# Kernel tuning notes

Hardware: AMD Instinct MI355X
Metric: run time of the kernel (lower is better)

## Reference

```python
import jax, jax.numpy as jnp
import numpy as np

HID = 128
OUT = 128
NC = 100000
NA = 1024
FC = 256
FA = 4096

def _sage(x_src, x_dst, ei, Wl, bl, Wr):
    # PyG SAGEConv, mean aggregation, bipartite:
    # out[i] = lin_l(mean_{j->i} x_src[j]) + lin_r(x_dst[i])
    n_dst = x_dst.shape[0]
    src, dst = ei[0], ei[1]
    msg = x_src[src]                                  # [E, F_src] gather
    agg = jax.ops.segment_sum(msg, dst, num_segments=n_dst)
    cnt = jax.ops.segment_sum(jnp.ones((ei.shape[1],), x_src.dtype), dst, num_segments=n_dst)
    mean = agg / jnp.clip(cnt, 1.0, None)[:, None]
    return mean @ Wl.T + bl + x_dst @ Wr.T

def setup_inputs() -> dict:
    key = jax.random.key(0)
    ks = jax.random.split(key, 20)
    d = {}
    d["article_x"] = jax.random.normal(ks[0], (1, FA), jnp.float32)
    d["community_x"] = jax.random.normal(ks[1], (NC, FC), jnp.float32)
    # bipartite edges: row = article node idx (<NA), col = community idx (<NC)
    d["e_wb"] = jnp.stack([jax.random.randint(ks[2], (500000,), 0, NA, jnp.int32),
                            jax.random.randint(ks[3], (500000,), 0, NC, jnp.int32)])
    d["e_mb"] = jnp.stack([jax.random.randint(ks[4], (500000,), 0, NA, jnp.int32),
                            jax.random.randint(ks[5], (500000,), 0, NC, jnp.int32)])
    d["e_cc"] = jax.random.randint(ks[6], (2, 800000), 0, NC, jnp.int32)
    s = lambda k, sh: jax.random.normal(k, sh, jnp.float32) * (1.0 / np.sqrt(sh[-1]))
    d["W_lin1"] = s(ks[7], (NA, FA)); d["b_lin1"] = jnp.zeros((NA,), jnp.float32)
    d["Wl1"] = s(ks[8], (HID, 1));   d["bl1"] = jnp.zeros((HID,), jnp.float32); d["Wr1"] = s(ks[9], (HID, FC))
    d["Wl2"] = s(ks[10], (HID, 1));  d["bl2"] = jnp.zeros((HID,), jnp.float32); d["Wr2"] = s(ks[11], (HID, HID))
    d["Wl3"] = s(ks[12], (HID, HID)); d["bl3"] = jnp.zeros((HID,), jnp.float32); d["Wr3"] = s(ks[13], (HID, FC))
    d["W_lin2"] = s(ks[14], (OUT, HID)); d["b_lin2"] = jnp.zeros((OUT,), jnp.float32)
    d["Wd1"] = s(ks[15], (OUT, 2 * OUT)); d["bd1"] = jnp.zeros((OUT,), jnp.float32)
    d["Wd2"] = s(ks[16], (1, OUT)); d["bd2"] = jnp.zeros((1,), jnp.float32)
    return d

def reference(article_x, community_x, e_wb, e_mb, e_cc,
              W_lin1, b_lin1, Wl1, bl1, Wr1, Wl2, bl2, Wr2,
              Wl3, bl3, Wr3, W_lin2, b_lin2, Wd1, bd1, Wd2, bd2):
    # encoder
    art = (article_x @ W_lin1.T + b_lin1).reshape(NA, 1)      # [1024, 1]
    h1 = jax.nn.relu(_sage(art, community_x, e_wb, Wl1, bl1, Wr1))   # [NC, HID]
    h2 = jax.nn.relu(_sage(art, h1, e_mb, Wl2, bl2, Wr2))            # [NC, HID]
    h3 = jax.nn.relu(_sage(h2, community_x, e_cc, Wl3, bl3, Wr3))    # [NC, HID]
    z = h3 @ W_lin2.T + b_lin2                                       # [NC, OUT]
    # edge decoder on interacts_with edges
    row, col = e_cc[0], e_cc[1]
    zz = jnp.concatenate([z[row], z[col]], axis=-1)                  # [E, 2*OUT]
    h = jax.nn.relu(zz @ Wd1.T + bd1)
    return (h @ Wd2.T + bd2).reshape(-1)                             # [E]
```

## Files before the change

### kernel.cpp

```cpp
#include <hip/hip_runtime.h>

#define NC 100000
#define NA 1024
#define FA 4096

typedef _Float16 half8 __attribute__((ext_vector_type(8)));
typedef _Float16 half4v __attribute__((ext_vector_type(4)));
typedef _Float16 half2v __attribute__((ext_vector_type(2)));
typedef float floatx4 __attribute__((ext_vector_type(4)));

#define CNT_OFF 4294967296.0
#define CNT_INV 2.3283064365386963e-10

__device__ __forceinline__ void cvt_range(const float* __restrict__ in,
                                          _Float16* __restrict__ out, int n4,
                                          int bid, int nb) {
    int t = bid * 256 + threadIdx.x;
    int stride = nb * 256;
    for (int i = t; i < n4; i += stride) {
        float4 v = ((const float4*)in)[i];
        half4v h = {(_Float16)v.x, (_Float16)v.y, (_Float16)v.z, (_Float16)v.w};
        ((half4v*)out)[i] = h;
    }
}

__device__ __forceinline__ void edge_seg(const int* __restrict__ ei, int E,
                                         const float* __restrict__ art,
                                         double* __restrict__ acd, int bid, int nb) {
    int t = bid * 256 + threadIdx.x;
    int stride = nb * 256;
    for (int e = t; e < E; e += stride) {
        int s = ei[e], d = ei[E + e];
        atomicAdd(&acd[d], (double)art[s] + CNT_OFF);
    }
}

__device__ __forceinline__ void hist_seg(const int* __restrict__ ei, int E,
                                         int* __restrict__ deg, int bid, int nb) {
    int t = bid * 256 + threadIdx.x;
    int stride = nb * 256;
    for (int e = t; e < E; e += stride) atomicAdd(&deg[ei[E + e]], 1);
}

__device__ __forceinline__ void wcomb_seg(const float* __restrict__ Wd1,
                                          const float* __restrict__ Wlin2,
                                          _Float16* __restrict__ Wuh,
                                          _Float16* __restrict__ Wvh, int bid) {
    int i = bid * 2 + (threadIdx.x >> 7);
    int j = threadIdx.x & 127;
    float au = 0.f, av = 0.f;
    for (int m = 0; m < 128; ++m) {
        float wl = Wlin2[m * 128 + j];
        au = fmaf(Wd1[i * 256 + m], wl, au);
        av = fmaf(Wd1[i * 256 + 128 + m], wl, av);
    }
    Wuh[i * 128 + j] = (_Float16)au;
    Wvh[i * 128 + j] = (_Float16)av;
}

__device__ __forceinline__ void bcomb_seg(const float* __restrict__ Wd1,
                                          const float* __restrict__ b2,
                                          const float* __restrict__ bd1,
                                          float* __restrict__ bu, float* __restrict__ bv) {
    int i = threadIdx.x;
    if (i >= 128) return;
    float su = 0.f, sv = 0.f;
    for (int m = 0; m < 128; ++m) {
        float b = b2[m];
        su = fmaf(Wd1[i * 256 + m], b, su);
        sv = fmaf(Wd1[i * 256 + 128 + m], b, sv);
    }
    bu[i] = su + bd1[i];
    bv[i] = sv;
}

#define FRONT_WB   1024
#define FRONT_MB   1024
#define FRONT_HIST 768
#define FRONT_WCVT 96
#define FRONT_WCOMB 64
#define FRONT_BCOMB 1
#define FRONT_CVT  8192
#define FRONT_TOTAL (FRONT_WB + FRONT_MB + FRONT_HIST + FRONT_WCVT + FRONT_WCOMB + FRONT_BCOMB + FRONT_CVT)

__global__ __launch_bounds__(256)
void k_front(const int* __restrict__ e_wb, int E1,
             const int* __restrict__ e_mb, int E2,
             const int* __restrict__ e_cc, int E3,
             const float* __restrict__ art,
             double* __restrict__ acd1, double* __restrict__ acd2,
             int* __restrict__ deg,
             const float* __restrict__ Wr1, _Float16* __restrict__ Wr1h,
             const float* __restrict__ Wr2, _Float16* __restrict__ Wr2h,
             const float* __restrict__ Wl3, _Float16* __restrict__ Wl3h,
             const float* __restrict__ Wr3, _Float16* __restrict__ Wr3h,
             const float* __restrict__ Wd1, const float* __restrict__ Wlin2,
             _Float16* __restrict__ Wuh, _Float16* __restrict__ Wvh,
             const float* __restrict__ b2, const float* __restrict__ bd1,
             float* __restrict__ bu, float* __restrict__ bv,
             const float* __restrict__ cx, _Float16* __restrict__ cxh)
{
    int b = blockIdx.x;
    if (b < FRONT_WB) { edge_seg(e_wb, E1, art, acd1, b, FRONT_WB); return; }
    b -= FRONT_WB;
    if (b < FRONT_MB) { edge_seg(e_mb, E2, art, acd2, b, FRONT_MB); return; }
    b -= FRONT_MB;
    if (b < FRONT_HIST) { hist_seg(e_cc, E3, deg, b, FRONT_HIST); return; }
    b -= FRONT_HIST;
    if (b < FRONT_WCVT) {
        if (b < 32) cvt_range(Wr1, Wr1h, 8192, b, 32);
        else if (b < 48) cvt_range(Wr2, Wr2h, 4096, b - 32, 16);
        else if (b < 64) cvt_range(Wl3, Wl3h, 4096, b - 48, 16);
        else cvt_range(Wr3, Wr3h, 8192, b - 64, 32);
        return;
    }
    b -= FRONT_WCVT;
    if (b < FRONT_WCOMB) { wcomb_seg(Wd1, Wlin2, Wuh, Wvh, b); return; }
    b -= FRONT_WCOMB;
    if (b < FRONT_BCOMB) { bcomb_seg(Wd1, b2, bd1, bu, bv); return; }
    b -= FRONT_BCOMB;
    cvt_range(cx, cxh, NC * 64, b, FRONT_CVT);
}

__global__ void k_art(const float* __restrict__ ax, const float* __restrict__ W,
                      const float* __restrict__ b, float* __restrict__ art) {
    int wave = (blockIdx.x * blockDim.x + threadIdx.x) >> 6;
    int lane = threadIdx.x & 63;
    if (wave >= NA) return;
    const float* wr = W + (size_t)wave * FA;
    float s = 0.f;
    #pragma unroll
    for (int i = 0; i < FA; i += 256) {
        float4 a  = *(const float4*)&ax[i + 4 * lane];
        float4 wv = *(const float4*)&wr[i + 4 * lane];
        s += a.x * wv.x + a.y * wv.y + a.z * wv.z + a.w * wv.w;
    }
    for (int off = 32; off; off >>= 1) s += __shfl_down(s, off);
    if (lane == 0) art[wave] = s + b[wave];
}

__global__ void k_scan1(const int* __restrict__ deg, int* __restrict__ pre,
                        int* __restrict__ blksum) {
    __shared__ int ts[256];
    int base = blockIdx.x * 1024 + threadIdx.x * 4;
    int v0 = 0, v1 = 0, v2 = 0, v3 = 0;
    if (base + 0 < NC) v0 = deg[base + 0];
    if (base + 1 < NC) v1 = deg[base + 1];
    if (base + 2 < NC) v2 = deg[base + 2];
    if (base + 3 < NC) v3 = deg[base + 3];
    int tsum = v0 + v1 + v2 + v3;
    ts[threadIdx.x] = tsum;
    __syncthreads();
    for (int off = 1; off < 256; off <<= 1) {
        int y = (threadIdx.x >= off) ? ts[threadIdx.x - off] : 0;
        __syncthreads();
        ts[threadIdx.x] += y;
        __syncthreads();
    }
    int excl = ts[threadIdx.x] - tsum;
    if (base + 0 < NC) pre[base + 0] = excl;
    if (base + 1 < NC) pre[base + 1] = excl + v0;
    if (base + 2 < NC) pre[base + 2] = excl + v0 + v1;
    if (base + 3 < NC) pre[base + 3] = excl + v0 + v1 + v2;
    if (threadIdx.x == 255) blksum[blockIdx.x] = ts[255];
}

__global__ void k_scan2(int* __restrict__ blksum, int NB) {
    __shared__ int ts[256];
    int v = (threadIdx.x < NB) ? blksum[threadIdx.x] : 0;
    ts[threadIdx.x] = v;
    __syncthreads();
    for (int off = 1; off < 256; off <<= 1) {
        int y = (threadIdx.x >= off) ? ts[threadIdx.x - off] : 0;
        __syncthreads();
        ts[threadIdx.x] += y;
        __syncthreads();
    }
    if (threadIdx.x < NB) blksum[threadIdx.x] = ts[threadIdx.x] - v;
}

__global__ void k_scan3(const int* __restrict__ pre, const int* __restrict__ blksum,
                        const int* __restrict__ deg, int* __restrict__ off,
                        int* __restrict__ cursor, float* __restrict__ cntf) {
    int i = blockIdx.x * blockDim.x + threadIdx.x;
    if (i < NC) {
        int o = pre[i] + blksum[i >> 10];
        off[i] = o;
        cursor[i] = o;
        cntf[i] = (float)deg[i];
    }
}

__device__ __forceinline__ float mean_from_packed(double t) {
    double cd = rint(t * CNT_INV);
    float sum = (float)(t - cd * CNT_OFF);
    float cc = (float)cd;
    cc = cc > 1.f ? cc : 1.f;
    return sum / cc;
}

__device__ __forceinline__
void enc12_body(_Float16* lds, int blk,
                const _Float16* __restrict__ cxh, const _Float16* __restrict__ Wr1h,
                const _Float16* __restrict__ Wr2h,
                const float* __restrict__ bl1, const double* __restrict__ acd1,
                const float* __restrict__ Wl1,
                const float* __restrict__ bl2, const double* __restrict__ acd2,
                const float* __restrict__ Wl2,
                _Float16* __restrict__ out, int N)
{
    _Float16* Bh  = lds;
    _Float16* Ah  = lds + 128 * 40;
    _Float16* h1t = lds + 128 * 40;

    const int t = threadIdx.x, lane = t & 63, w = t >> 6;
    const int rowbase = blk * 128;
    const bool isA = t < 128;
    const int rr = isA ? t : t - 128;
    const int fr = lane & 15;
    const int kq = (lane >> 4) << 3;

    floatx4 zero4 = {0.f, 0.f, 0.f, 0.f};
    floatx4 acc[2][8];
    #pragma unroll
    for (int i = 0; i < 2; ++i)
        #pragma unroll
        for (int cf = 0; cf < 8; ++cf) acc[i][cf] = zero4;

    float4 p0, p1, p2, p3;
    float4 zf = make_float4(0.f, 0.f, 0.f, 0.f);
    {
        bool ok = true; const _Float16* base;
        if (isA) { int row = rowbase + rr; ok = row < N; base = ok ? &cxh[(size_t)row * 256] : Ah; }
        else base = &Wr1h[(size_t)rr * 256];
        const float4* s4 = (const float4*)base;
        p0 = ok ? s4[0] : zf; p1 = ok ? s4[1] : zf; p2 = ok ? s4[2] : zf; p3 = ok ? s4[3] : zf;
    }
    for (int tile = 0; tile < 8; ++tile) {
        float4* dst = (float4*)(isA ? &Ah[rr * 40] : &Bh[rr * 40]);
        dst[0] = p0; dst[1] = p1; dst[2] = p2; dst[3] = p3;
        __syncthreads();
        if (tile < 7) {
            int ko = (tile + 1) << 5;
            bool ok = true; const _Float16* base;
            if (isA) { int row = rowbase + rr; ok = row < N; base = ok ? &cxh[(size_t)row * 256 + ko] : Ah; }
            else base = &Wr1h[(size_t)rr * 256 + ko];
            const float4* s4 = (const float4*)base;
            p0 = ok ? s4[0] : zf; p1 = ok ? s4[1] : zf; p2 = ok ? s4[2] : zf; p3 = ok ? s4[3] : zf;
        }
        half8 af0 = *(const half8*)&Ah[(w * 32 + fr) * 40 + kq];
        half8 af1 = *(const half8*)&Ah[(w * 32 + 16 + fr) * 40 + kq];
        #pragma unroll
        for (int cf = 0; cf < 8; ++cf) {
            half8 bf = *(const half8*)&Bh[(cf * 16 + fr) * 40 + kq];
            acc[0][cf] = __builtin_amdgcn_mfma_f32_16x16x32_f16(af0, bf, acc[0][cf], 0, 0, 0);
            acc[1][cf] = __builtin_amdgcn_mfma_f32_16x16x32_f16(af1, bf, acc[1][cf], 0, 0, 0);
        }
        __syncthreads();
    }

    {
        float blc[8], wlc[8];
        #pragma unroll
        for (int cf = 0; cf < 8; ++cf) { int col = cf * 16 + fr; blc[cf] = bl1[col]; wlc[cf] = Wl1[col]; }
        #pragma unroll
        for (int i = 0; i < 2; ++i) {
            #pragma unroll
            for (int j = 0; j < 4; ++j) {
                int lrow = w * 32 + i * 16 + ((lane >> 4) << 2) + j;
                int grow = rowbase + lrow;
                float m = 0.f;
                if (grow < N) m = mean_from_packed(acd1[grow]);
                #pragma unroll
                for (int cf = 0; cf < 8; ++cf) {
                    float v = acc[i][cf][j] + blc[cf] + m * wlc[cf];
                    v = fmaxf(v, 0.f);
                    h1t[lrow * 136 + cf * 16 + fr] = (_Float16)v;
                }
            }
        }
    }
    __syncthreads();

    #pragma unroll
    for (int i = 0; i < 2; ++i)
        #pragma unroll
        for (int cf = 0; cf < 8; ++cf) acc[i][cf] = zero4;
    if (!isA) {
        const float4* s4 = (const float4*)&Wr2h[(size_t)rr * 128];
        p0 = s4[0]; p1 = s4[1]; p2 = s4[2]; p3 = s4[3];
    }
    for (int tt = 0; tt < 4; ++tt) {
        if (!isA) { float4* d = (float4*)&Bh[rr * 40]; d[0] = p0; d[1] = p1; d[2] = p2; d[3] = p3; }
        __syncthreads();
        if (!isA && tt < 3) {
            const float4* s4 = (const float4*)&Wr2h[(size_t)rr * 128 + ((tt + 1) << 5)];
            p0 = s4[0]; p1 = s4[1]; p2 = s4[2]; p3 = s4[3];
        }
        half8 af0 = *(const half8*)&h1t[(w * 32 + fr) * 136 + (tt << 5) + kq];
        half8 af1 = *(const half8*)&h1t[(w * 32 + 16 + fr) * 136 + (tt << 5) + kq];
        #pragma unroll
        for (int cf = 0; cf < 8; ++cf) {
            half8 bf = *(const half8*)&Bh[(cf * 16 + fr) * 40 + kq];
            acc[0][cf] = __builtin_amdgcn_mfma_f32_16x16x32_f16(af0, bf, acc[0][cf], 0, 0, 0);
            acc[1][cf] = __builtin_amdgcn_mfma_f32_16x16x32_f16(af1, bf, acc[1][cf], 0, 0, 0);
        }
        __syncthreads();
    }

    {
        float blc[8], wlc[8];
        #pragma unroll
        for (int cf = 0; cf < 8; ++cf) { int col = cf * 16 + fr; blc[cf] = bl2[col]; wlc[cf] = Wl2[col]; }
        #pragma unroll
        for (int i = 0; i < 2; ++i) {
            #pragma unroll
            for (int j = 0; j < 4; ++j) {
                int grow = rowbase + w * 32 + i * 16 + ((lane >> 4) << 2) + j;
                if (grow < N) {
                    float m = mean_from_packed(acd2[grow]);
                    #pragma unroll
                    for (int cf = 0; cf < 8; ++cf) {
                        float v = acc[i][cf][j] + blc[cf] + m * wlc[cf];
                        v = fmaxf(v, 0.f);
                        out[(size_t)grow * 128 + cf * 16 + fr] = (_Float16)v;
                    }
                }
            }
        }
    }
}

#define MID_GB  ((NC + 127) / 128)
#define MID_SC  768

__global__ __launch_bounds__(256)
void k_mid(const _Float16* __restrict__ cxh, const _Float16* __restrict__ Wr1h,
           const _Float16* __restrict__ Wr2h,
           const float* __restrict__ bl1, const double* __restrict__ acd1,
           const float* __restrict__ Wl1,
           const float* __restrict__ bl2, const double* __restrict__ acd2,
           const float* __restrict__ Wl2,
           _Float16* __restrict__ out, int N,
           const int* __restrict__ e_cc, int E3,
           int* __restrict__ cursor, int2* __restrict__ se)
{
    __shared__ _Float16 lds[128 * 40 + 128 * 136];
    if (blockIdx.x < MID_GB) {
        enc12_body(lds, blockIdx.x, cxh, Wr1h, Wr2h, bl1, acd1, Wl1, bl2, acd2, Wl2, out, N);
        return;
    }
    int bid = blockIdx.x - MID_GB;
    int t = bid * 256 + threadIdx.x;
    int stride = MID_SC * 256;
    for (int e = t; e < E3; e += stride) {
        int s = e_cc[e], d = e_cc[E3 + e];
        int p = atomicAdd(&cursor[d], 1);
        se[p] = make_int2(s, e);
    }
}

__global__ __launch_bounds__(256)
void k_csr_agg_h(const int* __restrict__ off, const int* __restrict__ deg,
                 const int2* __restrict__ se, const _Float16* __restrict__ h,
                 _Float16* __restrict__ agg) {
    int node = (blockIdx.x * blockDim.x + threadIdx.x) >> 6;
    int lane = threadIdx.x & 63;
    if (node >= NC) return;
    int b = off[node], d = deg[node];
    int dm = d < 64 ? d : 64;
    int sj = 0;
    if (lane < dm) sj = se[b + lane].x;
    float sx = 0.f, sy = 0.f;
    #pragma unroll 4
    for (int j = 0; j < dm; ++j) {
        int src = __shfl(sj, j);
        half2v m = *(const half2v*)&h[(size_t)src * 128 + 2 * lane];
        sx += (float)m[0]; sy += (float)m[1];
    }
    for (int j = 64; j < d; ++j) {
        int src = se[b + j].x;
        half2v m = *(const half2v*)&h[(size_t)src * 128 + 2 * lane];
        sx += (float)m[0]; sy += (float)m[1];
    }
    half2v r = {(_Float16)sx, (_Float16)sy};
    *(half2v*)&agg[(size_t)node * 128 + 2 * lane] = r;
}

__global__ __launch_bounds__(256)
void k_enc3uv(const _Float16* __restrict__ aggh, const _Float16* __restrict__ Wl3h,
              const _Float16* __restrict__ cxh, const _Float16* __restrict__ Wr3h,
              const float* __restrict__ bl3, const float* __restrict__ rcnt,
              const _Float16* __restrict__ Wuh, const float* __restrict__ bu,
              const _Float16* __restrict__ Wvh, const float* __restrict__ bv,
              _Float16* __restrict__ uout, _Float16* __restrict__ vout, int N)
{
    __shared__ _Float16 lds[128 * 40 + 128 * 136];
    _Float16* Bh  = lds;
    _Float16* Ah  = lds + 128 * 40;
    _Float16* h3t = lds + 128 * 40;

    const int t = threadIdx.x, lane = t & 63, w = t >> 6;
    const int rowbase = blockIdx.x * 128;
    const bool isA = t < 128;
    const int rr = isA ? t : t - 128;
    const int fr = lane & 15;
    const int kq = (lane >> 4) << 3;

    floatx4 zero4 = {0.f, 0.f, 0.f, 0.f};
    floatx4 acc[2][8];
    #pragma unroll
    for (int i = 0; i < 2; ++i)
        #pragma unroll
        for (int cf = 0; cf < 8; ++cf) acc[i][cf] = zero4;

    float4 p0, p1, p2, p3;
    float4 zf = make_float4(0.f, 0.f, 0.f, 0.f);
    {
        bool ok = true; const _Float16* base;
        if (isA) { int row = rowbase + rr; ok = row < N; base = ok ? &aggh[(size_t)row * 128] : Ah; }
        else base = &Wl3h[(size_t)rr * 128];
        const float4* s4 = (const float4*)base;
        p0 = ok ? s4[0] : zf; p1 = ok ? s4[1] : zf; p2 = ok ? s4[2] : zf; p3 = ok ? s4[3] : zf;
    }
    for (int tile = 0; tile < 12; ++tile) {
        float4* dst = (float4*)(isA ? &Ah[rr * 40] : &Bh[rr * 40]);
        dst[0] = p0; dst[1] = p1; dst[2] = p2; dst[3] = p3;
        __syncthreads();
        if (tile < 11) {
            int tn = tile + 1;
            bool ok = true; const _Float16* base;
            if (tn < 4) {
                int ko = tn << 5;
                if (isA) { int row = rowbase + rr; ok = row < N; base = ok ? &aggh[(size_t)row * 128 + ko] : Ah; }
                else base = &Wl3h[(size_t)rr * 128 + ko];
            } else {
                int ko = (tn - 4) << 5;
                if (isA) { int row = rowbase + rr; ok = row < N; base = ok ? &cxh[(size_t)row * 256 + ko] : Ah; }
                else base = &Wr3h[(size_t)rr * 256 + ko];
            }
            const float4* s4 = (const float4*)base;
            p0 = ok ? s4[0] : zf; p1 = ok ? s4[1] : zf; p2 = ok ? s4[2] : zf; p3 = ok ? s4[3] : zf;
        }
        half8 af0 = *(const half8*)&Ah[(w * 32 + fr) * 40 + kq];
        half8 af1 = *(const half8*)&Ah[(w * 32 + 16 + fr) * 40 + kq];
        #pragma unroll
        for (int cf = 0; cf < 8; ++cf) {
            half8 bf = *(const half8*)&Bh[(cf * 16 + fr) * 40 + kq];
            acc[0][cf] = __builtin_amdgcn_mfma_f32_16x16x32_f16(af0, bf, acc[0][cf], 0, 0, 0);
            acc[1][cf] = __builtin_amdgcn_mfma_f32_16x16x32_f16(af1, bf, acc[1][cf], 0, 0, 0);
        }
        if (tile == 3) {
            #pragma unroll
            for (int i = 0; i < 2; ++i)
                #pragma unroll
                for (int j = 0; j < 4; ++j) {
                    int row = rowbase + w * 32 + i * 16 + ((lane >> 4) << 2) + j;
                    float c = (row < N) ? rcnt[row] : 1.f;
                    c = c > 1.f ? c : 1.f;
                    float inv = 1.f / c;
                    #pragma unroll
                    for (int cf = 0; cf < 8; ++cf) acc[i][cf][j] *= inv;
                }
        }
        __syncthreads();
    }

    {
        float blc[8];
        #pragma unroll
        for (int cf = 0; cf < 8; ++cf) blc[cf] = bl3[cf * 16 + fr];
        #pragma unroll
        for (int i = 0; i < 2; ++i) {
            #pragma unroll
            for (int j = 0; j < 4; ++j) {
                int lrow = w * 32 + i * 16 + ((lane >> 4) << 2) + j;
                #pragma unroll
                for (int cf = 0; cf < 8; ++cf) {
                    float v = acc[i][cf][j] + blc[cf];
                    v = fmaxf(v, 0.f);
                    h3t[lrow * 136 + cf * 16 + fr] = (_Float16)v;
                }
            }
        }
    }
    __syncthreads();

    for (int ph = 0; ph < 2; ++ph) {
        const _Float16* Wp = ph ? Wvh : Wuh;
        const float* bp = ph ? bv : bu;
        _Float16* op = ph ? vout : uout;
        #pragma unroll
        for (int i = 0; i < 2; ++i)
            #pragma unroll
            for (int cf = 0; cf < 8; ++cf) acc[i][cf] = zero4;
        if (!isA) {
            const float4* s4 = (const float4*)&Wp[(size_t)rr * 128];
            p0 = s4[0]; p1 = s4[1]; p2 = s4[2]; p3 = s4[3];
        }
        for (int tt = 0; tt < 4; ++tt) {
            if (!isA) { float4* d = (float4*)&Bh[rr * 40]; d[0] = p0; d[1] = p1; d[2] = p2; d[3] = p3; }
            __syncthreads();
            if (!isA && tt < 3) {
                const float4* s4 = (const float4*)&Wp[(size_t)rr * 128 + ((tt + 1) << 5)];
                p0 = s4[0]; p1 = s4[1]; p2 = s4[2]; p3 = s4[3];
            }
            half8 af0 = *(const half8*)&h3t[(w * 32 + fr) * 136 + (tt << 5) + kq];
            half8 af1 = *(const half8*)&h3t[(w * 32 + 16 + fr) * 136 + (tt << 5) + kq];
            #pragma unroll
            for (int cf = 0; cf < 8; ++cf) {
                half8 bf = *(const half8*)&Bh[(cf * 16 + fr) * 40 + kq];
                acc[0][cf] = __builtin_amdgcn_mfma_f32_16x16x32_f16(af0, bf, acc[0][cf], 0, 0, 0);
                acc[1][cf] = __builtin_amdgcn_mfma_f32_16x16x32_f16(af1, bf, acc[1][cf], 0, 0, 0);
            }
            __syncthreads();
        }
        float bc[8];
        #pragma unroll
        for (int cf = 0; cf < 8; ++cf) bc[cf] = bp[cf * 16 + fr];
        #pragma unroll
        for (int i = 0; i < 2; ++i) {
            #pragma unroll
            for (int j = 0; j < 4; ++j) {
                int grow = rowbase + w * 32 + i * 16 + ((lane >> 4) << 2) + j;
                if (grow < N) {
                    #pragma unroll
                    for (int cf = 0; cf < 8; ++cf)
                        op[(size_t)grow * 128 + cf * 16 + fr] = (_Float16)(acc[i][cf][j] + bc[cf]);
                }
            }
        }
    }
}

__global__ __launch_bounds__(256)
void k_decoder_h(const int* __restrict__ off, const int* __restrict__ deg,
                 const int2* __restrict__ se,
                 const _Float16* __restrict__ u, const _Float16* __restrict__ v,
                 const float* __restrict__ wd2, const float* __restrict__ bd2,
                 float* __restrict__ out) {
    int node = (blockIdx.x * blockDim.x + threadIdx.x) >> 6;
    if (node >= NC) return;
    int lane = threadIdx.x & 63;
    int g = lane >> 3, s = lane & 7;

    float wf[16], vf[16];
    #pragma unroll
    for (int q = 0; q < 16; ++q) wf[q] = wd2[s * 16 + q];
    {
        half8 va = *(const half8*)&v[(size_t)node * 128 + s * 16];
        half8 vb = *(const half8*)&v[(size_t)node * 128 + s * 16 + 8];
        #pragma unroll
        for (int q = 0; q < 8; ++q) { vf[q] = (float)va[q]; vf[8 + q] = (float)vb[q]; }
    }
    float bb = bd2[0];

    int b = off[node], d = deg[node];
    int dm = d < 64 ? d : 64;
    int sj = 0, ej = 0;
    if (lane < dm) { int2 p = se[b + lane]; sj = p.x; ej = p.y; }

    for (int jb = 0; jb < d; jb += 8) {
        int j = jb + g;
        float p = 0.f;
        int eid = 0;
        bool act = j < d;
        int src = 0;
        if (jb < 64) {
            src = __shfl(sj, j);
            eid = __shfl(ej, j);
        } else if (act) {
            int2 pr = se[b + j];
            src = pr.x; eid = pr.y;
        }
        if (act) {
            half8 ua = *(const half8*)&u[(size_t)src * 128 + s * 16];
            half8 ub = *(const half8*)&u[(size_t)src * 128 + s * 16 + 8];
            #pragma unroll
            for (int q = 0; q < 8; ++q) {
                p = fmaf(wf[q],     fmaxf((float)ua[q] + vf[q],     0.f), p);
                p = fmaf(wf[8 + q], fmaxf((float)ub[q] + vf[8 + q], 0.f), p);
            }
        }
        p += __shfl_xor(p, 1);
        p += __shfl_xor(p, 2);
        p += __shfl_xor(p, 4);
        if (act && s == 0) out[eid] = p + bb;
    }
}

extern "C" void kernel_launch(void* const* d_in, const int* in_sizes, int n_in,
                              void* d_out, int out_size, void* d_ws, size_t ws_size,
                              hipStream_t stream) {
    const float* article_x = (const float*)d_in[0];
    const float* cx     = (const float*)d_in[1];
    const int*   e_wb   = (const int*)d_in[2];
    const int*   e_mb   = (const int*)d_in[3];
    const int*   e_cc   = (const int*)d_in[4];
    const float* W_lin1 = (const float*)d_in[5];
    const float* b_lin1 = (const float*)d_in[6];
    const float* Wl1    = (const float*)d_in[7];
    const float* bl1    = (const float*)d_in[8];
    const float* Wr1    = (const float*)d_in[9];
    const float* Wl2    = (const float*)d_in[10];
    const float* bl2    = (const float*)d_in[11];
    const float* Wr2    = (const float*)d_in[12];
    const float* Wl3    = (const float*)d_in[13];
    const float* bl3    = (const float*)d_in[14];
    const float* Wr3    = (const float*)d_in[15];
    const float* W_lin2 = (const float*)d_in[16];
    const float* b_lin2 = (const float*)d_in[17];
    const float* Wd1    = (const float*)d_in[18];
    const float* bd1    = (const float*)d_in[19];
    const float* Wd2    = (const float*)d_in[20];
    const float* bd2    = (const float*)d_in[21];
    float* out = (float*)d_out;

    const int E1 = in_sizes[2] / 2;
    const int E2 = in_sizes[3] / 2;
    const int E3 = in_sizes[4] / 2;

    double* acd1 = (double*)d_ws;
    double* acd2 = acd1 + NC;
    float* ws = (float*)(acd2 + NC);
    size_t o = 0;
    float* art   = ws;      o += 1024;
    float* cnt3f = ws + o;  o += NC;
    float* buf   = ws + o;  o += 128;
    float* bvf   = ws + o;  o += 128;
    int* deg    = (int*)(ws + o); o += NC;
    int* pre    = (int*)(ws + o); o += NC;
    int* off    = (int*)(ws + o); o += NC;
    int* cursor = (int*)(ws + o); o += NC;
    int* blksum = (int*)(ws + o); o += 256;
    int2* se    = (int2*)(ws + o); o += 2 * 800000;
    _Float16* hws = (_Float16*)(ws + o);
    size_t ho = 0;
    _Float16* cxh    = hws + ho; ho += (size_t)NC * 256;
    _Float16* B1h    = hws + ho; ho += (size_t)NC * 128;
    _Float16* B2h    = hws + ho; ho += (size_t)NC * 128;
    _Float16* Wr1h   = hws + ho; ho += 128 * 256;
    _Float16* Wr2h   = hws + ho; ho += 128 * 128;
    _Float16* Wl3h   = hws + ho; ho += 128 * 128;
    _Float16* Wr3h   = hws + ho; ho += 128 * 256;
    _Float16* Wuh    = hws + ho; ho += 128 * 128;
    _Float16* Wvh    = hws + ho; ho += 128 * 128;

    hipMemsetAsync(acd1, 0, 2 * NC * sizeof(double), stream);
    hipMemsetAsync(deg, 0, NC * sizeof(int), stream);

    k_art<<<256, 256, 0, stream>>>(article_x, W_lin1, b_lin1, art);

    k_front<<<FRONT_TOTAL, 256, 0, stream>>>(
        e_wb, E1, e_mb, E2, e_cc, E3, art, acd1, acd2, deg,
        Wr1, Wr1h, Wr2, Wr2h, Wl3, Wl3h, Wr3, Wr3h,
        Wd1, W_lin2, Wuh, Wvh, b_lin2, bd1, buf, bvf, cx, cxh);

    const int NB = (NC + 1023) / 1024;
    k_scan1<<<NB, 256, 0, stream>>>(deg, pre, blksum);
    k_scan2<<<1, 256, 0, stream>>>(blksum, NB);
    k_scan3<<<(NC + 255) / 256, 256, 0, stream>>>(pre, blksum, deg, off, cursor, cnt3f);

    k_mid<<<MID_GB + MID_SC, 256, 0, stream>>>(
        cxh, Wr1h, Wr2h, bl1, acd1, Wl1, bl2, acd2, Wl2,
        B1h, NC, e_cc, E3, cursor, se);

    const int GW = (NC * 64 + 255) / 256;
    k_csr_agg_h<<<GW, 256, 0, stream>>>(off, deg, se, B1h, B2h);
    k_enc3uv<<<MID_GB, 256, 0, stream>>>(B2h, Wl3h, cxh, Wr3h,
                                         bl3, cnt3f, Wuh, buf, Wvh, bvf,
                                         B1h, B2h, NC);
    k_decoder_h<<<GW, 256, 0, stream>>>(off, deg, se, B1h, B2h, Wd2, bd2, out);
}
```

Before: 349.6 us.

## Regroup front kernels and schedule CSR scatter blocks first in mid kernel

```diff
diff --git a/kernel.cpp b/kernel.cpp
--- a/kernel.cpp
+++ b/kernel.cpp
@@ -74,57 +74,11 @@
     bv[i] = sv;
 }
 
-#define FRONT_WB   1024
-#define FRONT_MB   1024
-#define FRONT_HIST 768
-#define FRONT_WCVT 96
-#define FRONT_WCOMB 64
-#define FRONT_BCOMB 1
-#define FRONT_CVT  8192
-#define FRONT_TOTAL (FRONT_WB + FRONT_MB + FRONT_HIST + FRONT_WCVT + FRONT_WCOMB + FRONT_BCOMB + FRONT_CVT)
-
-__global__ __launch_bounds__(256)
-void k_front(const int* __restrict__ e_wb, int E1,
-             const int* __restrict__ e_mb, int E2,
-             const int* __restrict__ e_cc, int E3,
-             const float* __restrict__ art,
-             double* __restrict__ acd1, double* __restrict__ acd2,
-             int* __restrict__ deg,
-             const float* __restrict__ Wr1, _Float16* __restrict__ Wr1h,
-             const float* __restrict__ Wr2, _Float16* __restrict__ Wr2h,
-             const float* __restrict__ Wl3, _Float16* __restrict__ Wl3h,
-             const float* __restrict__ Wr3, _Float16* __restrict__ Wr3h,
-             const float* __restrict__ Wd1, const float* __restrict__ Wlin2,
-             _Float16* __restrict__ Wuh, _Float16* __restrict__ Wvh,
-             const float* __restrict__ b2, const float* __restrict__ bd1,
-             float* __restrict__ bu, float* __restrict__ bv,
-             const float* __restrict__ cx, _Float16* __restrict__ cxh)
-{
-    int b = blockIdx.x;
-    if (b < FRONT_WB) { edge_seg(e_wb, E1, art, acd1, b, FRONT_WB); return; }
-    b -= FRONT_WB;
-    if (b < FRONT_MB) { edge_seg(e_mb, E2, art, acd2, b, FRONT_MB); return; }
-    b -= FRONT_MB;
-    if (b < FRONT_HIST) { hist_seg(e_cc, E3, deg, b, FRONT_HIST); return; }
-    b -= FRONT_HIST;
-    if (b < FRONT_WCVT) {
-        if (b < 32) cvt_range(Wr1, Wr1h, 8192, b, 32);
-        else if (b < 48) cvt_range(Wr2, Wr2h, 4096, b - 32, 16);
-        else if (b < 64) cvt_range(Wl3, Wl3h, 4096, b - 48, 16);
-        else cvt_range(Wr3, Wr3h, 8192, b - 64, 32);
-        return;
-    }
-    b -= FRONT_WCVT;
-    if (b < FRONT_WCOMB) { wcomb_seg(Wd1, Wlin2, Wuh, Wvh, b); return; }
-    b -= FRONT_WCOMB;
-    if (b < FRONT_BCOMB) { bcomb_seg(Wd1, b2, bd1, bu, bv); return; }
-    b -= FRONT_BCOMB;
-    cvt_range(cx, cxh, NC * 64, b, FRONT_CVT);
-}
-
-__global__ void k_art(const float* __restrict__ ax, const float* __restrict__ W,
-                      const float* __restrict__ b, float* __restrict__ art) {
-    int wave = (blockIdx.x * blockDim.x + threadIdx.x) >> 6;
+__device__ __forceinline__ void art_seg(const float* __restrict__ ax,
+                                        const float* __restrict__ W,
+                                        const float* __restrict__ b,
+                                        float* __restrict__ art, int bid) {
+    int wave = (bid * 256 + threadIdx.x) >> 6;
     int lane = threadIdx.x & 63;
     if (wave >= NA) return;
     const float* wr = W + (size_t)wave * FA;
@@ -137,6 +91,64 @@
     }
     for (int off = 32; off; off >>= 1) s += __shfl_down(s, off);
     if (lane == 0) art[wave] = s + b[wave];
+}
+
+#define PRE_ART   256
+#define PRE_HIST  512
+#define PRE_WCVT  96
+#define PRE_WCOMB 64
+#define PRE_BCOMB 1
+#define PRE_CVT   4096
+#define PRE_TOTAL (PRE_ART + PRE_HIST + PRE_WCVT + PRE_WCOMB + PRE_BCOMB + PRE_CVT)
+
+__global__ __launch_bounds__(256)
+void k_pre(const float* __restrict__ ax, const float* __restrict__ W_lin1,
+           const float* __restrict__ b_lin1, float* __restrict__ art,
+           const int* __restrict__ e_cc, int E3, int* __restrict__ deg,
+           const float* __restrict__ Wr1, _Float16* __restrict__ Wr1h,
+           const float* __restrict__ Wr2, _Float16* __restrict__ Wr2h,
+           const float* __restrict__ Wl3, _Float16* __restrict__ Wl3h,
+           const float* __restrict__ Wr3, _Float16* __restrict__ Wr3h,
+           const float* __restrict__ Wd1, const float* __restrict__ Wlin2,
+           _Float16* __restrict__ Wuh, _Float16* __restrict__ Wvh,
+           const float* __restrict__ b2, const float* __restrict__ bd1,
+           float* __restrict__ bu, float* __restrict__ bv,
+           const float* __restrict__ cx, _Float16* __restrict__ cxh)
+{
+    int b = blockIdx.x;
+    if (b < PRE_ART) { art_seg(ax, W_lin1, b_lin1, art, b); return; }
+    b -= PRE_ART;
+    if (b < PRE_HIST) { hist_seg(e_cc, E3, deg, b, PRE_HIST); return; }
+    b -= PRE_HIST;
+    if (b < PRE_WCVT) {
+        if (b < 32) cvt_range(Wr1, Wr1h, 8192, b, 32);
+        else if (b < 48) cvt_range(Wr2, Wr2h, 4096, b - 32, 16);
+        else if (b < 64) cvt_range(Wl3, Wl3h, 4096, b - 48, 16);
+        else cvt_range(Wr3, Wr3h, 8192, b - 64, 32);
+        return;
+    }
+    b -= PRE_WCVT;
+    if (b < PRE_WCOMB) { wcomb_seg(Wd1, Wlin2, Wuh, Wvh, b); return; }
+    b -= PRE_WCOMB;
+    if (b < PRE_BCOMB) { bcomb_seg(Wd1, b2, bd1, bu, bv); return; }
+    b -= PRE_BCOMB;
+    cvt_range(cx, cxh, NC * 64, b, PRE_CVT);
+}
+
+#define EDG_WB 1024
+#define EDG_MB 1024
+#define EDG_TOTAL (EDG_WB + EDG_MB)
+
+__global__ __launch_bounds__(256)
+void k_edges(const int* __restrict__ e_wb, int E1,
+             const int* __restrict__ e_mb, int E2,
+             const float* __restrict__ art,
+             double* __restrict__ acd1, double* __restrict__ acd2)
+{
+    int b = blockIdx.x;
+    if (b < EDG_WB) { edge_seg(e_wb, E1, art, acd1, b, EDG_WB); return; }
+    b -= EDG_WB;
+    edge_seg(e_mb, E2, art, acd2, b, EDG_MB);
 }
 
 __global__ void k_scan1(const int* __restrict__ deg, int* __restrict__ pre,
@@ -331,8 +343,8 @@
     }
 }
 
+#define MID_SC  256
 #define MID_GB  ((NC + 127) / 128)
-#define MID_SC  768
 
 __global__ __launch_bounds__(256)
 void k_mid(const _Float16* __restrict__ cxh, const _Float16* __restrict__ Wr1h,
@@ -346,18 +358,18 @@
            int* __restrict__ cursor, int2* __restrict__ se)
 {
     __shared__ _Float16 lds[128 * 40 + 128 * 136];
-    if (blockIdx.x < MID_GB) {
-        enc12_body(lds, blockIdx.x, cxh, Wr1h, Wr2h, bl1, acd1, Wl1, bl2, acd2, Wl2, out, N);
+    if (blockIdx.x < MID_SC) {
+        int t = blockIdx.x * 256 + threadIdx.x;
+        int stride = MID_SC * 256;
+        #pragma unroll 4
+        for (int e = t; e < E3; e += stride) {
+            int s = e_cc[e], d = e_cc[E3 + e];
+            int p = atomicAdd(&cursor[d], 1);
+            se[p] = make_int2(s, e);
+        }
         return;
     }
-    int bid = blockIdx.x - MID_GB;
-    int t = bid * 256 + threadIdx.x;
-    int stride = MID_SC * 256;
-    for (int e = t; e < E3; e += stride) {
-        int s = e_cc[e], d = e_cc[E3 + e];
-        int p = atomicAdd(&cursor[d], 1);
-        se[p] = make_int2(s, e);
-    }
+    enc12_body(lds, blockIdx.x - MID_SC, cxh, Wr1h, Wr2h, bl1, acd1, Wl1, bl2, acd2, Wl2, out, N);
 }
 
 __global__ __launch_bounds__(256)
@@ -649,19 +661,20 @@
     hipMemsetAsync(acd1, 0, 2 * NC * sizeof(double), stream);
     hipMemsetAsync(deg, 0, NC * sizeof(int), stream);
 
-    k_art<<<256, 256, 0, stream>>>(article_x, W_lin1, b_lin1, art);
-
-    k_front<<<FRONT_TOTAL, 256, 0, stream>>>(
-        e_wb, E1, e_mb, E2, e_cc, E3, art, acd1, acd2, deg,
+    k_pre<<<PRE_TOTAL, 256, 0, stream>>>(
+        article_x, W_lin1, b_lin1, art,
+        e_cc, E3, deg,
         Wr1, Wr1h, Wr2, Wr2h, Wl3, Wl3h, Wr3, Wr3h,
         Wd1, W_lin2, Wuh, Wvh, b_lin2, bd1, buf, bvf, cx, cxh);
+
+    k_edges<<<EDG_TOTAL, 256, 0, stream>>>(e_wb, E1, e_mb, E2, art, acd1, acd2);
 
     const int NB = (NC + 1023) / 1024;
     k_scan1<<<NB, 256, 0, stream>>>(deg, pre, blksum);
     k_scan2<<<1, 256, 0, stream>>>(blksum, NB);
     k_scan3<<<(NC + 255) / 256, 256, 0, stream>>>(pre, blksum, deg, off, cursor, cnt3f);
 
-    k_mid<<<MID_GB + MID_SC, 256, 0, stream>>>(
+    k_mid<<<MID_SC + MID_GB, 256, 0, stream>>>(
         cxh, Wr1h, Wr2h, bl1, acd1, Wl1, bl2, acd2, Wl2,
         B1h, NC, e_cc, E3, cursor, se);
 
```

Measured after the change: 365.6 us. +4.6%, slower.

## Replicate atomic accumulators across eight copies and reduce them in the scan kernel

Applied to the files above, without the earlier changes.

```diff
diff --git a/kernel.cpp b/kernel.cpp
--- a/kernel.cpp
+++ b/kernel.cpp
@@ -3,6 +3,7 @@
 #define NC 100000
 #define NA 1024
 #define FA 4096
+#define NREP 8
 
 typedef _Float16 half8 __attribute__((ext_vector_type(8)));
 typedef _Float16 half4v __attribute__((ext_vector_type(4)));
@@ -72,54 +73,6 @@
     }
     bu[i] = su + bd1[i];
     bv[i] = sv;
-}
-
-#define FRONT_WB   1024
-#define FRONT_MB   1024
-#define FRONT_HIST 768
-#define FRONT_WCVT 96
-#define FRONT_WCOMB 64
-#define FRONT_BCOMB 1
-#define FRONT_CVT  8192
-#define FRONT_TOTAL (FRONT_WB + FRONT_MB + FRONT_HIST + FRONT_WCVT + FRONT_WCOMB + FRONT_BCOMB + FRONT_CVT)
-
-__global__ __launch_bounds__(256)
-void k_front(const int* __restrict__ e_wb, int E1,
-             const int* __restrict__ e_mb, int E2,
-             const int* __restrict__ e_cc, int E3,
-             const float* __restrict__ art,
-             double* __restrict__ acd1, double* __restrict__ acd2,
-             int* __restrict__ deg,
-             const float* __restrict__ Wr1, _Float16* __restrict__ Wr1h,
-             const float* __restrict__ Wr2, _Float16* __restrict__ Wr2h,
-             const float* __restrict__ Wl3, _Float16* __restrict__ Wl3h,
-             const float* __restrict__ Wr3, _Float16* __restrict__ Wr3h,
-             const float* __restrict__ Wd1, const float* __restrict__ Wlin2,
-             _Float16* __restrict__ Wuh, _Float16* __restrict__ Wvh,
-             const float* __restrict__ b2, const float* __restrict__ bd1,
-             float* __restrict__ bu, float* __restrict__ bv,
-             const float* __restrict__ cx, _Float16* __restrict__ cxh)
-{
-    int b = blockIdx.x;
-    if (b < FRONT_WB) { edge_seg(e_wb, E1, art, acd1, b, FRONT_WB); return; }
-    b -= FRONT_WB;
-    if (b < FRONT_MB) { edge_seg(e_mb, E2, art, acd2, b, FRONT_MB); return; }
-    b -= FRONT_MB;
-    if (b < FRONT_HIST) { hist_seg(e_cc, E3, deg, b, FRONT_HIST); return; }
-    b -= FRONT_HIST;
-    if (b < FRONT_WCVT) {
-        if (b < 32) cvt_range(Wr1, Wr1h, 8192, b, 32);
-        else if (b < 48) cvt_range(Wr2, Wr2h, 4096, b - 32, 16);
-        else if (b < 64) cvt_range(Wl3, Wl3h, 4096, b - 48, 16);
-        else cvt_range(Wr3, Wr3h, 8192, b - 64, 32);
-        return;
-    }
-    b -= FRONT_WCVT;
-    if (b < FRONT_WCOMB) { wcomb_seg(Wd1, Wlin2, Wuh, Wvh, b); return; }
-    b -= FRONT_WCOMB;
-    if (b < FRONT_BCOMB) { bcomb_seg(Wd1, b2, bd1, bu, bv); return; }
-    b -= FRONT_BCOMB;
-    cvt_range(cx, cxh, NC * 64, b, FRONT_CVT);
 }
 
 __global__ void k_art(const float* __restrict__ ax, const float* __restrict__ W,
@@ -139,15 +92,97 @@
     if (lane == 0) art[wave] = s + b[wave];
 }
 
-__global__ void k_scan1(const int* __restrict__ deg, int* __restrict__ pre,
-                        int* __restrict__ blksum) {
+#define FRONT_WB   1024
+#define FRONT_MB   1024
+#define FRONT_HIST 768
+#define FRONT_WCVT 96
+#define FRONT_WCOMB 64
+#define FRONT_BCOMB 1
+#define FRONT_CVT  8192
+#define FRONT_TOTAL (FRONT_WB + FRONT_MB + FRONT_HIST + FRONT_WCVT + FRONT_WCOMB + FRONT_BCOMB + FRONT_CVT)
+
+__global__ __launch_bounds__(256)
+void k_front(const int* __restrict__ e_wb, int E1,
+             const int* __restrict__ e_mb, int E2,
+             const int* __restrict__ e_cc, int E3,
+             const float* __restrict__ art,
+             double* __restrict__ acdr1, double* __restrict__ acdr2,
+             int* __restrict__ degr,
+             const float* __restrict__ Wr1, _Float16* __restrict__ Wr1h,
+             const float* __restrict__ Wr2, _Float16* __restrict__ Wr2h,
+             const float* __restrict__ Wl3, _Float16* __restrict__ Wl3h,
+             const float* __restrict__ Wr3, _Float16* __restrict__ Wr3h,
+             const float* __restrict__ Wd1, const float* __restrict__ Wlin2,
+             _Float16* __restrict__ Wuh, _Float16* __restrict__ Wvh,
+             const float* __restrict__ b2, const float* __restrict__ bd1,
+             float* __restrict__ bu, float* __restrict__ bv,
+             const float* __restrict__ cx, _Float16* __restrict__ cxh)
+{
+    int b = blockIdx.x;
+    if (b < FRONT_WB) { edge_seg(e_wb, E1, art, acdr1 + (size_t)(b & (NREP-1)) * NC, b, FRONT_WB); return; }
+    b -= FRONT_WB;
+    if (b < FRONT_MB) { edge_seg(e_mb, E2, art, acdr2 + (size_t)(b & (NREP-1)) * NC, b, FRONT_MB); return; }
+    b -= FRONT_MB;
+    if (b < FRONT_HIST) { hist_seg(e_cc, E3, degr + (size_t)(b & (NREP-1)) * NC, b, FRONT_HIST); return; }
+    b -= FRONT_HIST;
+    if (b < FRONT_WCVT) {
+        if (b < 32) cvt_range(Wr1, Wr1h, 8192, b, 32);
+        else if (b < 48) cvt_range(Wr2, Wr2h, 4096, b - 32, 16);
+        else if (b < 64) cvt_range(Wl3, Wl3h, 4096, b - 48, 16);
+        else cvt_range(Wr3, Wr3h, 8192, b - 64, 32);
+        return;
+    }
+    b -= FRONT_WCVT;
+    if (b < FRONT_WCOMB) { wcomb_seg(Wd1, Wlin2, Wuh, Wvh, b); return; }
+    b -= FRONT_WCOMB;
+    if (b < FRONT_BCOMB) { bcomb_seg(Wd1, b2, bd1, bu, bv); return; }
+    b -= FRONT_BCOMB;
+    cvt_range(cx, cxh, NC * 64, b, FRONT_CVT);
+}
+
+#define S1R_SCAN 98
+#define S1R_RED  ((2 * NC + 255) / 256)
+#define S1R_TOTAL (S1R_SCAN + S1R_RED)
+
+__global__ __launch_bounds__(256)
+void k_scan1red(const int* __restrict__ degr, int* __restrict__ deg,
+                int* __restrict__ pre, int* __restrict__ blksum,
+                const double* __restrict__ acdr1, double* __restrict__ acd1,
+                const double* __restrict__ acdr2, double* __restrict__ acd2)
+{
+    if (blockIdx.x >= S1R_SCAN) {
+        int i = (blockIdx.x - S1R_SCAN) * 256 + threadIdx.x;
+        if (i < NC) {
+            double s = 0.0;
+            #pragma unroll
+            for (int r = 0; r < NREP; ++r) s += acdr1[(size_t)r * NC + i];
+            acd1[i] = s;
+        } else {
+            int j = i - NC;
+            if (j < NC) {
+                double s = 0.0;
+                #pragma unroll
+                for (int r = 0; r < NREP; ++r) s += acdr2[(size_t)r * NC + j];
+                acd2[j] = s;
+            }
+        }
+        return;
+    }
     __shared__ int ts[256];
     int base = blockIdx.x * 1024 + threadIdx.x * 4;
     int v0 = 0, v1 = 0, v2 = 0, v3 = 0;
-    if (base + 0 < NC) v0 = deg[base + 0];
-    if (base + 1 < NC) v1 = deg[base + 1];
-    if (base + 2 < NC) v2 = deg[base + 2];
-    if (base + 3 < NC) v3 = deg[base + 3];
+    #pragma unroll
+    for (int r = 0; r < NREP; ++r) {
+        const int* dr = degr + (size_t)r * NC;
+        if (base + 0 < NC) v0 += dr[base + 0];
+        if (base + 1 < NC) v1 += dr[base + 1];
+        if (base + 2 < NC) v2 += dr[base + 2];
+        if (base + 3 < NC) v3 += dr[base + 3];
+    }
+    if (base + 0 < NC) deg[base + 0] = v0;
+    if (base + 1 < NC) deg[base + 1] = v1;
+    if (base + 2 < NC) deg[base + 2] = v2;
+    if (base + 3 < NC) deg[base + 3] = v3;
     int tsum = v0 + v1 + v2 + v3;
     ts[threadIdx.x] = tsum;
     __syncthreads();
@@ -331,8 +366,8 @@
     }
 }
 
+#define MID_SC  256
 #define MID_GB  ((NC + 127) / 128)
-#define MID_SC  768
 
 __global__ __launch_bounds__(256)
 void k_mid(const _Float16* __restrict__ cxh, const _Float16* __restrict__ Wr1h,
@@ -346,18 +381,18 @@
            int* __restrict__ cursor, int2* __restrict__ se)
 {
     __shared__ _Float16 lds[128 * 40 + 128 * 136];
-    if (blockIdx.x < MID_GB) {
-        enc12_body(lds, blockIdx.x, cxh, Wr1h, Wr2h, bl1, acd1, Wl1, bl2, acd2, Wl2, out, N);
+    if (blockIdx.x < MID_SC) {
+        int t = blockIdx.x * 256 + threadIdx.x;
+        int stride = MID_SC * 256;
+        #pragma unroll 4
+        for (int e = t; e < E3; e += stride) {
+            int s = e_cc[e], d = e_cc[E3 + e];
+            int p = atomicAdd(&cursor[d], 1);
+            se[p] = make_int2(s, e);
+        }
         return;
     }
-    int bid = blockIdx.x - MID_GB;
-    int t = bid * 256 + threadIdx.x;
-    int stride = MID_SC * 256;
-    for (int e = t; e < E3; e += stride) {
-        int s = e_cc[e], d = e_cc[E3 + e];
-        int p = atomicAdd(&cursor[d], 1);
-        se[p] = make_int2(s, e);
-    }
+    enc12_body(lds, blockIdx.x - MID_SC, cxh, Wr1h, Wr2h, bl1, acd1, Wl1, bl2, acd2, Wl2, out, N);
 }
 
 __global__ __launch_bounds__(256)
@@ -646,22 +681,26 @@
     _Float16* Wuh    = hws + ho; ho += 128 * 128;
     _Float16* Wvh    = hws + ho; ho += 128 * 128;
 
-    hipMemsetAsync(acd1, 0, 2 * NC * sizeof(double), stream);
-    hipMemsetAsync(deg, 0, NC * sizeof(int), stream);
+    double* acdr1 = (double*)B1h;
+    double* acdr2 = acdr1 + (size_t)NREP * NC;
+    int*    degr  = (int*)B2h;
+
+    hipMemsetAsync(acdr1, 0, (size_t)2 * NREP * NC * sizeof(double), stream);
+    hipMemsetAsync(degr, 0, (size_t)NREP * NC * sizeof(int), stream);
 
     k_art<<<256, 256, 0, stream>>>(article_x, W_lin1, b_lin1, art);
 
     k_front<<<FRONT_TOTAL, 256, 0, stream>>>(
-        e_wb, E1, e_mb, E2, e_cc, E3, art, acd1, acd2, deg,
+        e_wb, E1, e_mb, E2, e_cc, E3, art, acdr1, acdr2, degr,
         Wr1, Wr1h, Wr2, Wr2h, Wl3, Wl3h, Wr3, Wr3h,
         Wd1, W_lin2, Wuh, Wvh, b_lin2, bd1, buf, bvf, cx, cxh);
 
-    const int NB = (NC + 1023) / 1024;
-    k_scan1<<<NB, 256, 0, stream>>>(deg, pre, blksum);
-    k_scan2<<<1, 256, 0, stream>>>(blksum, NB);
+    k_scan1red<<<S1R_TOTAL, 256, 0, stream>>>(degr, deg, pre, blksum,
+                                              acdr1, acd1, acdr2, acd2);
+    k_scan2<<<1, 256, 0, stream>>>(blksum, S1R_SCAN);
     k_scan3<<<(NC + 255) / 256, 256, 0, stream>>>(pre, blksum, deg, off, cursor, cnt3f);
 
-    k_mid<<<MID_GB + MID_SC, 256, 0, stream>>>(
+    k_mid<<<MID_SC + MID_GB, 256, 0, stream>>>(
         cxh, Wr1h, Wr2h, bl1, acd1, Wl1, bl2, acd2, Wl2,
         B1h, NC, e_cc, E3, cursor, se);
 
```

Measured after the change: 359.2 us. 2.7% more time.
